# Kernel optimization log

Measured on AMD Instinct MI355X. Metric: run time of the kernel, lower is better.

## Reference

```python
import jax, jax.numpy as jnp
import numpy as np

NEG = -1e30  # effective -inf in float32, safe under logaddexp grads
EPS = 1e-7   # keras.backend.epsilon()


def _ctc_loss(y_pred, y_true):
    """Faithful port of keras.backend.ctc_batch_cost with full-length
    input_length=T and label_length=L (as the CTCLayer sets them).
    y_pred: [B, T, C] post-softmax probabilities; blank = C-1.
    y_true: [B, L] int labels in [0, C-1).
    Returns loss [B, 1].
    """
    logp = jnp.log(y_pred + EPS)            # keras takes log(prob + eps)
    B, T, C = y_pred.shape
    L = y_true.shape[1]
    S = 2 * L + 1
    blank = C - 1

    # Extended label sequence: blank, l1, blank, l2, ..., blank  -> [B, S]
    ext = jnp.full((B, S), blank, dtype=y_true.dtype).at[:, 1::2].set(y_true)
    # Per-time emission log-probs of extended symbols: [B, T, S]
    lp_ext = jnp.take_along_axis(logp, ext[:, None, :], axis=2)

    # Skip transition s-2 -> s allowed when ext[s] != blank and ext[s] != ext[s-2]
    prev2_ext = jnp.pad(ext[:, :-2], ((0, 0), (2, 0)), constant_values=-1)
    allow_skip = (ext != blank) & (ext != prev2_ext)  # [B, S]

    # alpha init at t=0
    alpha = jnp.full((B, S), NEG, dtype=logp.dtype)
    alpha = alpha.at[:, 0].set(lp_ext[:, 0, 0]).at[:, 1].set(lp_ext[:, 0, 1])

    def step(alpha, lp_t):
        shift1 = jnp.pad(alpha[:, :-1], ((0, 0), (1, 0)), constant_values=NEG)
        shift2 = jnp.pad(alpha[:, :-2], ((0, 0), (2, 0)), constant_values=NEG)
        shift2 = jnp.where(allow_skip, shift2, NEG)
        new = jnp.logaddexp(jnp.logaddexp(alpha, shift1), shift2) + lp_t
        return new, None

    lp_seq = jnp.moveaxis(lp_ext[:, 1:, :], 1, 0)  # [T-1, B, S]
    alpha, _ = jax.lax.scan(step, alpha, lp_seq)

    # Terminate in final blank or final label
    loss = -jnp.logaddexp(alpha[:, S - 1], alpha[:, S - 2])  # [B]
    return loss[:, None]  # keras returns [B, 1]


def setup_inputs() -> dict:
    key = jax.random.key(0)
    k1, k2 = jax.random.split(key)
    B, T, C, L = 256, 256, 1000, 64
    y_true = jax.random.randint(k1, (B, L), 0, C - 1, dtype=jnp.int64)
    logits = jax.random.normal(k2, (B, T, C), dtype=jnp.float32)
    y_pred = jax.nn.softmax(logits, axis=-1)  # module expects softmax probs
    return {"y_true": y_true, "y_pred": y_pred}


def reference(y_true, y_pred):
    return _ctc_loss(y_pred, y_true)
```

## Files before the change

### kernel.cpp

```cpp
#include <hip/hip_runtime.h>


#define T_    256
#define C_    1000
#define L_    64
#define BLANK 999
#define EPSF  (1e-7f)
#define RS    68
#define NCHUNK ((T_ * RS) / 256)

__global__ __launch_bounds__(256)
void ctc_gather_kernel(const int* __restrict__ y_true,
                       const float* __restrict__ y_pred,
                       float* __restrict__ V) {
    const int wave = threadIdx.x >> 6;
    const int lane = threadIdx.x & 63;
    const int pair = blockIdx.x * 4 + wave;
    const int b = pair >> 8;

    const int lab = y_true[b * L_ + lane];
    const float* __restrict__ row = y_pred + (size_t)pair * C_;
    float* __restrict__ orow = V + (size_t)pair * RS;

    orow[1 + lane] = row[lab] + EPSF;
    if (lane == 0) orow[0] = row[BLANK] + EPSF;
}

__global__ __launch_bounds__(64)
void ctc_scan_kernel(const int* __restrict__ y_true,
                     const float* __restrict__ V,
                     float* __restrict__ out) {
    __shared__ float sb[T_ * RS];

    const int b    = blockIdx.x;
    const int lane = threadIdx.x;

    const float* __restrict__ strip = V + (size_t)b * T_ * RS;

#if __has_builtin(__builtin_amdgcn_global_load_lds)
    typedef const __attribute__((address_space(1))) float gfloat;
    typedef __attribute__((address_space(3))) float sfloat;
    #pragma unroll
    for (int k = 0; k < NCHUNK; ++k) {
        __builtin_amdgcn_global_load_lds((gfloat*)(strip + k * 256 + lane * 4),
                                         (sfloat*)(sb + k * 256), 16, 0, 0);
    }
    asm volatile("s_waitcnt vmcnt(0)" ::: "memory");
#else
    #pragma unroll
    for (int k = 0; k < NCHUNK; ++k)
        ((float4*)sb)[k * 64 + lane] = ((const float4*)strip)[k * 64 + lane];
    __syncthreads();
#endif

    const int lab   = y_true[b * L_ + lane];
    const int labm1 = __shfl_up(lab, 1, 64);
    const bool allow = (lane > 0) && (lab != labm1);

    float aE = 0.f, aO = 0.f, aL = 0.f, lsum = 0.f;
    if (lane == 0) { aE = sb[0]; aO = sb[1]; }

    float rB[4], rL[4];
    #pragma unroll
    for (int k = 0; k < 4; ++k) {
        rB[k] = sb[(1 + k) * RS];
        rL[k] = sb[(1 + k) * RS + 1 + lane];
    }

    for (int t0 = 1; t0 < T_; t0 += 4) {
        #pragma unroll
        for (int j = 0; j < 4; ++j) {
            const int t = t0 + j;
            if (t >= T_) break;
            const float pB = rB[j], pL = rL[j];
            int tn = t + 4; if (tn > T_ - 1) tn = T_ - 1;
            rB[j] = sb[tn * RS];
            rL[j] = sb[tn * RS + 1 + lane];

            float upO = __shfl_up(aO, 1, 64);
            if (lane == 0) upO = 0.f;

            const float nE = (aE + upO) * pB;
            const float sk = allow ? upO : 0.f;
            const float nO = (aO + aE + sk) * pL;
            const float nL = (aL + aO) * pB;
            aE = nE; aO = nO; aL = nL;

            if ((t & 7) == 0) {
                float m = fmaxf(fmaxf(aE, aO), aL);
                #pragma unroll
                for (int d = 1; d < 64; d <<= 1)
                    m = fmaxf(m, __shfl_xor(m, d, 64));
                const float r = __builtin_amdgcn_rcpf(m);
                aE *= r; aO *= r; aL *= r;
                lsum += __logf(m);
            }
        }
    }

    if (lane == 63) {
        out[b] = -(__logf(aL + aO) + lsum);
    }
}

extern "C" void kernel_launch(void* const* d_in, const int* in_sizes, int n_in,
                              void* d_out, int out_size, void* d_ws, size_t ws_size,
                              hipStream_t stream) {
    const int*   y_true = (const int*)d_in[0];
    const float* y_pred = (const float*)d_in[1];
    float*       out    = (float*)d_out;
    float*       V      = (float*)d_ws;
    (void)in_sizes; (void)n_in; (void)ws_size; (void)out_size;

    ctc_gather_kernel<<<dim3((256 * T_) / 4), dim3(256), 0, stream>>>(y_true, y_pred, V);
    ctc_scan_kernel<<<dim3(256), dim3(64), 0, stream>>>(y_true, V, out);
}
```

Before: 375.9 us.

## Fuse gather and scan into one kernel with producer waves prefetching time chunks

Merges the gather and scan kernels into a single 256-thread block per batch element. Wave 0 runs the alpha recursion over 64-step time chunks while waves 1-3 gather the next chunk's label and blank probabilities from global memory straight into LDS, and a barrier separates the chunks. This removes the workspace round trip and the second launch, and overlaps the gather with the serial scan. The cost is only 256 blocks of 256 threads, so the gather parallelism is far lower than the old 16K-block gather kernel.

```diff
diff --git a/kernel.cpp b/kernel.cpp
--- a/kernel.cpp
+++ b/kernel.cpp
@@ -7,98 +7,108 @@
 #define BLANK 999
 #define EPSF  (1e-7f)
 #define RS    68
-#define NCHUNK ((T_ * RS) / 256)
+#define CHUNK 64
 
 __global__ __launch_bounds__(256)
-void ctc_gather_kernel(const int* __restrict__ y_true,
-                       const float* __restrict__ y_pred,
-                       float* __restrict__ V) {
+void ctc_fused_kernel(const int* __restrict__ y_true,
+                      const float* __restrict__ y_pred,
+                      float* __restrict__ out) {
+    __shared__ float sb[T_ * RS];
+
     const int wave = threadIdx.x >> 6;
     const int lane = threadIdx.x & 63;
-    const int pair = blockIdx.x * 4 + wave;
-    const int b = pair >> 8;
+    const int b    = blockIdx.x;
 
     const int lab = y_true[b * L_ + lane];
-    const float* __restrict__ row = y_pred + (size_t)pair * C_;
-    float* __restrict__ orow = V + (size_t)pair * RS;
+    const float* __restrict__ base = y_pred + (size_t)b * T_ * C_;
 
-    orow[1 + lane] = row[lab] + EPSF;
-    if (lane == 0) orow[0] = row[BLANK] + EPSF;
-}
+    {
+        float v0[16];
+        #pragma unroll
+        for (int i = 0; i < 16; ++i)
+            v0[i] = base[(size_t)(wave + 4 * i) * C_ + lab];
+        #pragma unroll
+        for (int i = 0; i < 16; ++i)
+            sb[(wave + 4 * i) * RS + 1 + lane] = v0[i];
+        if (wave == 0)
+            sb[lane * RS] = base[(size_t)lane * C_ + BLANK];
+    }
+    __syncthreads();
 
-__global__ __launch_bounds__(64)
-void ctc_scan_kernel(const int* __restrict__ y_true,
-                     const float* __restrict__ V,
-                     float* __restrict__ out) {
-    __shared__ float sb[T_ * RS];
-
-    const int b    = blockIdx.x;
-    const int lane = threadIdx.x;
-
-    const float* __restrict__ strip = V + (size_t)b * T_ * RS;
-
-#if __has_builtin(__builtin_amdgcn_global_load_lds)
-    typedef const __attribute__((address_space(1))) float gfloat;
-    typedef __attribute__((address_space(3))) float sfloat;
-    #pragma unroll
-    for (int k = 0; k < NCHUNK; ++k) {
-        __builtin_amdgcn_global_load_lds((gfloat*)(strip + k * 256 + lane * 4),
-                                         (sfloat*)(sb + k * 256), 16, 0, 0);
-    }
-    asm volatile("s_waitcnt vmcnt(0)" ::: "memory");
-#else
-    #pragma unroll
-    for (int k = 0; k < NCHUNK; ++k)
-        ((float4*)sb)[k * 64 + lane] = ((const float4*)strip)[k * 64 + lane];
-    __syncthreads();
-#endif
-
-    const int lab   = y_true[b * L_ + lane];
     const int labm1 = __shfl_up(lab, 1, 64);
     const bool allow = (lane > 0) && (lab != labm1);
 
     float aE = 0.f, aO = 0.f, aL = 0.f, lsum = 0.f;
-    if (lane == 0) { aE = sb[0]; aO = sb[1]; }
+    float rB[4], rL[4];
 
-    float rB[4], rL[4];
-    #pragma unroll
     for (int k = 0; k < 4; ++k) {
-        rB[k] = sb[(1 + k) * RS];
-        rL[k] = sb[(1 + k) * RS + 1 + lane];
+        if (wave == 0) {
+            const int tA = (k == 0) ? 1 : k * CHUNK;
+            const int tB = k * CHUNK + CHUNK;
+            if (k == 0) {
+                aE = (lane == 0) ? sb[0] + EPSF : 0.f;
+                aO = (lane == 0) ? sb[1] + EPSF : 0.f;
+            }
+            #pragma unroll
+            for (int q = 0; q < 4; ++q) {
+                rB[q] = sb[(tA + q) * RS] + EPSF;
+                rL[q] = sb[(tA + q) * RS + 1 + lane] + EPSF;
+            }
+            for (int t0 = tA; t0 < tB; t0 += 4) {
+                #pragma unroll
+                for (int j = 0; j < 4; ++j) {
+                    const int t = t0 + j;
+                    if (t >= tB) break;
+                    const float pB = rB[j], pL = rL[j];
+                    const int tn = t + 4;
+                    if (tn < tB) {
+                        rB[j] = sb[tn * RS] + EPSF;
+                        rL[j] = sb[tn * RS + 1 + lane] + EPSF;
+                    }
+
+                    float upO = __shfl_up(aO, 1, 64);
+                    if (lane == 0) upO = 0.f;
+
+                    const float nE = (aE + upO) * pB;
+                    const float sk = allow ? upO : 0.f;
+                    const float nO = (aO + aE + sk) * pL;
+                    const float nL = (aL + aO) * pB;
+                    aE = nE; aO = nO; aL = nL;
+
+                    if ((t & 7) == 0) {
+                        float m = fmaxf(fmaxf(aE, aO), aL);
+                        #pragma unroll
+                        for (int d = 1; d < 64; d <<= 1)
+                            m = fmaxf(m, __shfl_xor(m, d, 64));
+                        const float r = __builtin_amdgcn_rcpf(m);
+                        aE *= r; aO *= r; aL *= r;
+                        lsum += __logf(m);
+                    }
+                }
+            }
+        } else if (k < 3) {
+            const int tC = (k + 1) * CHUNK;
+            const int r0 = wave - 1;
+            float v[22];
+            #pragma unroll
+            for (int i = 0; i < 22; ++i) {
+                const int r = r0 + 3 * i;
+                if (r < CHUNK)
+                    v[i] = base[(size_t)(tC + r) * C_ + lab];
+            }
+            #pragma unroll
+            for (int i = 0; i < 22; ++i) {
+                const int r = r0 + 3 * i;
+                if (r < CHUNK)
+                    sb[(tC + r) * RS + 1 + lane] = v[i];
+            }
+            if (wave == 1)
+                sb[(tC + lane) * RS] = base[(size_t)(tC + lane) * C_ + BLANK];
+        }
+        __syncthreads();
     }
 
-    for (int t0 = 1; t0 < T_; t0 += 4) {
-        #pragma unroll
-        for (int j = 0; j < 4; ++j) {
-            const int t = t0 + j;
-            if (t >= T_) break;
-            const float pB = rB[j], pL = rL[j];
-            int tn = t + 4; if (tn > T_ - 1) tn = T_ - 1;
-            rB[j] = sb[tn * RS];
-            rL[j] = sb[tn * RS + 1 + lane];
-
-            float upO = __shfl_up(aO, 1, 64);
-            if (lane == 0) upO = 0.f;
-
-            const float nE = (aE + upO) * pB;
-            const float sk = allow ? upO : 0.f;
-            const float nO = (aO + aE + sk) * pL;
-            const float nL = (aL + aO) * pB;
-            aE = nE; aO = nO; aL = nL;
-
-            if ((t & 7) == 0) {
-                float m = fmaxf(fmaxf(aE, aO), aL);
-                #pragma unroll
-                for (int d = 1; d < 64; d <<= 1)
-                    m = fmaxf(m, __shfl_xor(m, d, 64));
-                const float r = __builtin_amdgcn_rcpf(m);
-                aE *= r; aO *= r; aL *= r;
-                lsum += __logf(m);
-            }
-        }
-    }
-
-    if (lane == 63) {
+    if (wave == 0 && lane == 63) {
         out[b] = -(__logf(aL + aO) + lsum);
     }
 }
@@ -109,9 +119,7 @@
     const int*   y_true = (const int*)d_in[0];
     const float* y_pred = (const float*)d_in[1];
     float*       out    = (float*)d_out;
-    float*       V      = (float*)d_ws;
-    (void)in_sizes; (void)n_in; (void)ws_size; (void)out_size;
+    (void)in_sizes; (void)n_in; (void)d_ws; (void)ws_size; (void)out_size;
 
-    ctc_gather_kernel<<<dim3((256 * T_) / 4), dim3(256), 0, stream>>>(y_true, y_pred, V);
-    ctc_scan_kernel<<<dim3(256), dim3(64), 0, stream>>>(y_true, V, out);
+    ctc_fused_kernel<<<dim3(256), dim3(256), 0, stream>>>(y_true, y_pred, out);
 }
```

Measured after the change: 358.2 us. 4.7% less time.
